# Kernel optimization log

Measured on AMD Instinct MI355X. Metric: run time of the kernel, lower is better.

Reference implementation:

```python
import jax, jax.numpy as jnp
import numpy as np

B, N, D, H = 1, 1024, 128, 8
HD = (2 * D) // H  # head dim of the concatenated pair features


def setup_inputs() -> dict:
    key = jax.random.key(0)
    k1, k2, k3 = jax.random.split(key, 3)
    inp = jax.random.normal(k1, (B, N, D), dtype=jnp.float32)
    adj = jax.random.randint(k2, (B, N, N), 0, 2, dtype=jnp.int32)
    attn_weight = jax.random.normal(k3, (H, HD, 1), dtype=jnp.float32) * 0.02
    return {"inp": inp, "adj": adj, "attn_weight": attn_weight}


def reference(inp, adj, attn_weight):
    Bs, Ns, Ds = inp.shape
    # Faithful replication of the torch code, including the concat along dim 0
    # followed by a reshape (this mixes the two halves exactly as torch.view does
    # on the contiguous buffer).
    a = jnp.tile(inp, (1, 1, Ns)).reshape(Bs, Ns * Ns, Ds)   # src-broadcast half
    b = jnp.tile(inp, (1, Ns, 1))                            # dst-broadcast half (B, N*N, D)
    pair = jnp.concatenate([a, b], axis=0).reshape(Bs, Ns, Ns, H, HD)
    # (H, HD, 1) x (B, M, N, H, HD) -> (B, M, N); trailing o-axis of size 1 is summed out
    att = jnp.einsum('kho,bmnkh->bmn', attn_weight, pair)
    att = jnp.where(adj > 0, att, jnp.zeros((), att.dtype))  # masked_fill(mask==0, 0)
    att = jax.nn.softmax(jax.nn.leaky_relu(att, 0.01), axis=-1)
    # attn_drop is identity in eval mode
    return att
```

## Files before the change

### kernel.cpp

```cpp
#include <hip/hip_runtime.h>
#include <hip/hip_bf16.h>

#define NN 1024
#define DD 128


__global__ void prep_kernel(const float* __restrict__ inp,
                            const float* __restrict__ w,
                            float* __restrict__ alow,
                            float* __restrict__ z) {
    const int r = blockIdx.x;
    const int d = threadIdx.x;
    const float x = inp[r * DD + d];
    float pu = x * w[d];
    float pv = x * w[d + DD];
    #pragma unroll
    for (int off = 32; off > 0; off >>= 1) {
        pu += __shfl_down(pu, off);
        pv += __shfl_down(pv, off);
    }
    __shared__ float su[2], sv[2];
    const int wave = d >> 6;
    if ((d & 63) == 0) { su[wave] = pu; sv[wave] = pv; }
    __syncthreads();
    if (d == 0) {
        const float U = su[0] + su[1];
        const float V = sv[0] + sv[1];
        alow[r] = U + V;
        z[r]    = (r & 1) ? V : U;
    }
}

__global__ void __launch_bounds__(256)
row_kernel(const int* __restrict__ adj,
           const float* __restrict__ alow,
           const float* __restrict__ z,
           float* __restrict__ out) {
    const int m = blockIdx.x;
    const int t = threadIdx.x;

    const int4 a4 = ((const int4*)(adj + m * NN))[t];

    float raw[4];
    if (m < 512) {
        const float rv = (t < 128) ? alow[2 * m] : alow[2 * m + 1];
        raw[0] = raw[1] = raw[2] = raw[3] = rv;
    } else {
        const int tp = t & 127;
        const float4 za = ((const float4*)z)[2 * tp];
        const float4 zb = ((const float4*)z)[2 * tp + 1];
        raw[0] = za.x + za.y;
        raw[1] = za.z + za.w;
        raw[2] = zb.x + zb.y;
        raw[3] = zb.z + zb.w;
    }

    const int am[4] = {a4.x, a4.y, a4.z, a4.w};
    float e[4];
    float s = 0.f;
    #pragma unroll
    for (int i = 0; i < 4; ++i) {
        float x = (am[i] > 0) ? raw[i] : 0.0f;
        x = (x >= 0.0f) ? x : 0.01f * x;
        e[i] = __expf(x);
        s += e[i];
    }

    #pragma unroll
    for (int off = 32; off > 0; off >>= 1) s += __shfl_down(s, off);
    __shared__ float sm[4];
    if ((t & 63) == 0) sm[t >> 6] = s;
    __syncthreads();
    const float inv = 1.0f / (sm[0] + sm[1] + sm[2] + sm[3]);

    float4 o;
    o.x = e[0] * inv; o.y = e[1] * inv; o.z = e[2] * inv; o.w = e[3] * inv;
    ((float4*)(out + m * NN))[t] = o;
}

extern "C" void kernel_launch(void* const* d_in, const int* in_sizes, int n_in,
                              void* d_out, int out_size, void* d_ws, size_t ws_size,
                              hipStream_t stream) {
    const float* inp = (const float*)d_in[0];
    const int*   adj = (const int*)d_in[1];
    const float* w   = (const float*)d_in[2];
    float* out = (float*)d_out;

    float* alow = (float*)d_ws;
    float* z    = alow + NN;

    prep_kernel<<<NN, DD, 0, stream>>>(inp, w, alow, z);
    row_kernel<<<NN, 256, 0, stream>>>(adj, alow, z, out);
}
```

Before: 63.30 us.

## Precompute exponentials in prep kernel and use one thread per row dot product

```diff
diff --git a/kernel.cpp b/kernel.cpp
--- a/kernel.cpp
+++ b/kernel.cpp
@@ -5,73 +5,66 @@
 #define DD 128
 
 
-__global__ void prep_kernel(const float* __restrict__ inp,
-                            const float* __restrict__ w,
-                            float* __restrict__ alow,
-                            float* __restrict__ z) {
-    const int r = blockIdx.x;
-    const int d = threadIdx.x;
-    const float x = inp[r * DD + d];
-    float pu = x * w[d];
-    float pv = x * w[d + DD];
+__global__ void __launch_bounds__(128)
+prep_kernel(const float* __restrict__ inp,
+            const float* __restrict__ w,
+            float* __restrict__ eA,
+            float* __restrict__ eH) {
+    const int r = blockIdx.x * 128 + threadIdx.x;
+    const float4* row = (const float4*)(inp + r * DD);
+    const float4* wu4 = (const float4*)w;
+    const float4* wv4 = (const float4*)(w + DD);
+    float u = 0.f, v = 0.f;
     #pragma unroll
-    for (int off = 32; off > 0; off >>= 1) {
-        pu += __shfl_down(pu, off);
-        pv += __shfl_down(pv, off);
+    for (int k = 0; k < DD / 4; ++k) {
+        const float4 x  = row[k];
+        const float4 wu = wu4[k];
+        const float4 wv = wv4[k];
+        u += x.x * wu.x + x.y * wu.y + x.z * wu.z + x.w * wu.w;
+        v += x.x * wv.x + x.y * wv.y + x.z * wv.z + x.w * wv.w;
     }
-    __shared__ float su[2], sv[2];
-    const int wave = d >> 6;
-    if ((d & 63) == 0) { su[wave] = pu; sv[wave] = pv; }
-    __syncthreads();
-    if (d == 0) {
-        const float U = su[0] + su[1];
-        const float V = sv[0] + sv[1];
-        alow[r] = U + V;
-        z[r]    = (r & 1) ? V : U;
-    }
+    float slo = u + v;
+    slo = (slo >= 0.f) ? slo : 0.01f * slo;
+    eA[r] = __expf(slo);
+    const float zr = (r & 1) ? v : u;
+    const float zp = __shfl_xor(zr, 1);
+    float shi = zr + zp;
+    shi = (shi >= 0.f) ? shi : 0.01f * shi;
+    if ((r & 1) == 0) eH[r >> 1] = __expf(shi);
 }
 
 __global__ void __launch_bounds__(256)
 row_kernel(const int* __restrict__ adj,
-           const float* __restrict__ alow,
-           const float* __restrict__ z,
+           const float* __restrict__ eA,
+           const float* __restrict__ eH,
            float* __restrict__ out) {
     const int m = blockIdx.x;
     const int t = threadIdx.x;
 
     const int4 a4 = ((const int4*)(adj + m * NN))[t];
 
-    float raw[4];
+    float e[4];
     if (m < 512) {
-        const float rv = (t < 128) ? alow[2 * m] : alow[2 * m + 1];
-        raw[0] = raw[1] = raw[2] = raw[3] = rv;
+        const float ea = (t < 128) ? eA[2 * m] : eA[2 * m + 1];
+        e[0] = (a4.x > 0) ? ea : 1.0f;
+        e[1] = (a4.y > 0) ? ea : 1.0f;
+        e[2] = (a4.z > 0) ? ea : 1.0f;
+        e[3] = (a4.w > 0) ? ea : 1.0f;
     } else {
-        const int tp = t & 127;
-        const float4 za = ((const float4*)z)[2 * tp];
-        const float4 zb = ((const float4*)z)[2 * tp + 1];
-        raw[0] = za.x + za.y;
-        raw[1] = za.z + za.w;
-        raw[2] = zb.x + zb.y;
-        raw[3] = zb.z + zb.w;
+        const float4 eh = ((const float4*)eH)[t & 127];
+        e[0] = (a4.x > 0) ? eh.x : 1.0f;
+        e[1] = (a4.y > 0) ? eh.y : 1.0f;
+        e[2] = (a4.z > 0) ? eh.z : 1.0f;
+        e[3] = (a4.w > 0) ? eh.w : 1.0f;
     }
 
-    const int am[4] = {a4.x, a4.y, a4.z, a4.w};
-    float e[4];
-    float s = 0.f;
-    #pragma unroll
-    for (int i = 0; i < 4; ++i) {
-        float x = (am[i] > 0) ? raw[i] : 0.0f;
-        x = (x >= 0.0f) ? x : 0.01f * x;
-        e[i] = __expf(x);
-        s += e[i];
-    }
-
+    float s = (e[0] + e[1]) + (e[2] + e[3]);
     #pragma unroll
     for (int off = 32; off > 0; off >>= 1) s += __shfl_down(s, off);
     __shared__ float sm[4];
     if ((t & 63) == 0) sm[t >> 6] = s;
     __syncthreads();
-    const float inv = 1.0f / (sm[0] + sm[1] + sm[2] + sm[3]);
+    const float inv = 1.0f / ((sm[0] + sm[1]) + (sm[2] + sm[3]));
 
     float4 o;
     o.x = e[0] * inv; o.y = e[1] * inv; o.z = e[2] * inv; o.w = e[3] * inv;
@@ -86,9 +79,9 @@
     const float* w   = (const float*)d_in[2];
     float* out = (float*)d_out;
 
-    float* alow = (float*)d_ws;
-    float* z    = alow + NN;
+    float* eA = (float*)d_ws;
+    float* eH = eA + NN;
 
-    prep_kernel<<<NN, DD, 0, stream>>>(inp, w, alow, z);
-    row_kernel<<<NN, 256, 0, stream>>>(adj, alow, z, out);
+    prep_kernel<<<NN / 128, 128, 0, stream>>>(inp, w, eA, eH);
+    row_kernel<<<NN, 256, 0, stream>>>(adj, eA, eH, out);
 }
```

Result: slower. 64.78 us (+2.3%).
